# Optimization experiments

Measured on AMD Instinct MI355X. Metric: run time of the kernel, lower is better.

The kernel has to match this reference:

```python
import jax, jax.numpy as jnp
import numpy as np

EPS = 1e-5

def _layer_norm(x, g, b):
    mu = jnp.mean(x, axis=-1, keepdims=True)
    var = jnp.mean(jnp.square(x - mu), axis=-1, keepdims=True)
    return (x - mu) * jax.lax.rsqrt(var + EPS) * g + b

def setup_inputs() -> dict:
    key = jax.random.key(0)
    ks = jax.random.split(key, 12)
    B, N, K = 1, 4096, 64
    TD, P = 384, 128   # token_dim, pair_dim
    H = 2 * P          # transition hidden (expansion_factor_transition=2)
    x = jax.random.normal(ks[0], (B, N, TD), dtype=jnp.float32)
    pair_rep = jax.random.normal(ks[1], (B, N, K, P), dtype=jnp.float32)
    mask = jax.random.uniform(ks[2], (B, N)) > 0.1          # mostly valid residues
    neighbor_idx = jax.random.randint(ks[3], (B, N, K), 0, N, dtype=jnp.int32)
    slot_valid = jax.random.uniform(ks[4], (B, N, K)) > 0.1
    s = 0.02
    params = {
        'ln_g': jnp.ones((TD,), jnp.float32),
        'ln_b': jnp.zeros((TD,), jnp.float32),
        'Wx': jax.random.normal(ks[5], (TD, 2 * P), jnp.float32) * s,
        't_g': jnp.ones((P,), jnp.float32),
        't_b': jnp.zeros((P,), jnp.float32),
        'W1': jax.random.normal(ks[6], (P, H), jnp.float32) * s,
        'b1': jnp.zeros((H,), jnp.float32),
        'W2': jax.random.normal(ks[7], (H, P), jnp.float32) * s,
        'b2': jnp.zeros((P,), jnp.float32),
    }
    return dict(x=x, pair_rep=pair_rep, mask=mask, neighbor_idx=neighbor_idx,
                slot_valid=slot_valid, **params)

def _pair_transition(z, pair_mask, t_g, t_b, W1, b1, W2, b2):
    # OpenFold PairTransition: LN -> Linear -> ReLU -> Linear -> *mask
    h = _layer_norm(z, t_g, t_b)
    h = jax.nn.relu(jnp.einsum('bnkp,ph->bnkh', h, W1) + b1)
    out = jnp.einsum('bnkh,hp->bnkp', h, W2) + b2
    return out * pair_mask[..., None]

def reference(x, pair_rep, mask, neighbor_idx, slot_valid,
              ln_g, ln_b, Wx, t_g, t_b, W1, b1, W2, b2):
    B, N, K, P = pair_rep.shape
    mf = mask.astype(x.dtype)
    xm = x * mf[..., None]
    proj = jnp.einsum('bnt,tp->bnp', _layer_norm(xm, ln_g, ln_b), Wx)  # [B,N,2P]
    xp1, xp2 = proj[..., :P], proj[..., P:]
    flat_idx = neighbor_idx.reshape(B, N * K)
    # gather neighbor projections: xp1_j[b,n,k] = xp1[b, neighbor_idx[b,n,k]]
    xp1_j = jnp.take_along_axis(xp1, flat_idx[..., None], axis=1).reshape(B, N, K, P)
    nbr_valid = jnp.take_along_axis(mask, flat_idx, axis=1).reshape(B, N, K)
    pair_mask = (mask[:, :, None] & nbr_valid & slot_valid).astype(pair_rep.dtype)
    pair_rep = (pair_rep + xp2[:, :, None, :] + xp1_j) * pair_mask[..., None]
    pair_rep = pair_rep + _pair_transition(pair_rep, pair_mask, t_g, t_b, W1, b1, W2, b2)
    pair_rep = pair_rep * pair_mask[..., None]
    return pair_rep
```

## Files before the change

kernel.cpp:

```cpp
#include <hip/hip_runtime.h>
#include <stdint.h>

#define N_TOK 4096
#define TD 384
#define KNB 64
#define PD 128
#define HD 256
#define NPROJ 256
#define RPB 32
#define TPB_LN 16
#define TILES_PER_BLK 8

#define CAN_LN_G 0
#define CAN_LN_B 384
#define CAN_WX   768
#define CAN_T_G  99072
#define CAN_T_B  99200
#define CAN_W1   99328
#define CAN_B1   132096
#define CAN_W2   132352
#define CAN_B2   165120
#define CAN_TOTAL 165248

#define BW_OFF   663552
#define WXT_OFF  0
#define W1T_OFF  98304
#define W2T_OFF  131072
#define BW_TOTAL 163840
#define PROJ_OFF (1 << 20)

typedef __attribute__((ext_vector_type(8))) short bf16x8;
typedef __attribute__((ext_vector_type(4))) short s16x4;
typedef __attribute__((ext_vector_type(4))) float f32x4;
typedef __attribute__((ext_vector_type(2))) unsigned int u32x2;
typedef __attribute__((ext_vector_type(4))) unsigned int u32x4;

static __device__ __forceinline__ float bf2f(unsigned short u) {
    return __uint_as_float(((unsigned int)u) << 16);
}
static __device__ __forceinline__ unsigned short f2bf(float f) {
    unsigned int x = __float_as_uint(f);
    return (unsigned short)((x + 0x7FFFu + ((x >> 16) & 1u)) >> 16);
}
static __device__ __forceinline__ float loadf(const void* p, int mode, int i) {
    return mode ? bf2f(((const unsigned short*)p)[i]) : ((const float*)p)[i];
}
static __device__ __forceinline__ unsigned int flag_word(const void* p, int mode, int i) {
    if (mode == 0) return ((const unsigned int*)p)[i];
    if (mode == 1) return (unsigned int)((const unsigned char*)p)[i];
    if (mode == 2) return (unsigned int)((const unsigned short*)p)[i];
    return ((const unsigned int*)p)[i];
}
static __device__ __forceinline__ bool plaus16(unsigned int h) {
    if (h == 0u) return true;
    unsigned int e = (h >> 7) & 0xFFu;
    return (e >= 0x60u && e <= 0x9Fu);
}

__global__ __launch_bounds__(256) void detect_kernel(
        const void* __restrict__ x, const void* __restrict__ pair_rep,
        const void* __restrict__ mask, const void* __restrict__ slot,
        int* __restrict__ flags) {
    const int t = threadIdx.x;
    const int wave = t >> 6, lane = t & 63;
    if (wave < 2) {
        const unsigned int* w = (const unsigned int*)(wave == 0 ? x : pair_rep);
        unsigned int v = w[lane];
        bool pl = plaus16(v & 0xFFFFu) && plaus16(v >> 16);
        unsigned long long b = __ballot(pl);
        if (lane == 0) flags[2 + wave] = (__popcll(b) >= 56) ? 1 : 0;
    } else {
        const unsigned int* w = (const unsigned int*)(wave == 2 ? mask : slot);
        bool ok01 = true, okbf = true, anybf_lo = false;
        #pragma unroll
        for (int j = 0; j < 4; ++j) {
            unsigned int v = w[lane * 4 + j];
            if (v > 1u) ok01 = false;
            unsigned int h0 = v & 0xFFFFu, h1 = v >> 16;
            if (!(h0 == 0u || h0 == 0x3F80u)) okbf = false;
            if (!(h1 == 0u || h1 == 0x3F80u)) okbf = false;
            if (h0 == 0x3F80u) anybf_lo = true;
        }
        unsigned long long b01 = __ballot(ok01);
        unsigned long long bbf = __ballot(okbf);
        unsigned long long bev = __ballot(anybf_lo);
        if (lane == 0) {
            int mode;
            if (b01 == ~0ull) mode = 0;
            else if (bbf == ~0ull) mode = (bev != 0ull) ? 2 : 3;
            else mode = 1;
            flags[wave - 2] = mode;
        }
    }
}

__global__ __launch_bounds__(256) void prep_kernel(
        const void* p0, const void* p1, const void* p2, const void* p3,
        const void* p4, const void* p5, const void* p6, const void* p7,
        const void* p8, const int* __restrict__ flags,
        float* __restrict__ dstf, short* __restrict__ dstb) {
    const int mode = flags[2];
    int e = blockIdx.x * 256 + threadIdx.x;
    if (e < CAN_TOTAL) {
        const int offs[9] = {CAN_LN_G, CAN_LN_B, CAN_WX, CAN_T_G, CAN_T_B,
                             CAN_W1, CAN_B1, CAN_W2, CAN_B2};
        int s = 0;
        #pragma unroll
        for (int i = 1; i < 9; ++i) if (e >= offs[i]) s = i;
        const int local = e - offs[s];
        const void* p = (s == 0) ? p0 : (s == 1) ? p1 : (s == 2) ? p2 :
                        (s == 3) ? p3 : (s == 4) ? p4 : (s == 5) ? p5 :
                        (s == 6) ? p6 : (s == 7) ? p7 : p8;
        dstf[e] = loadf(p, mode, local);
    } else {
        int e2 = e - CAN_TOTAL;
        if (e2 >= BW_TOTAL) return;
        int src; const void* p;
        if (e2 < W1T_OFF)      { int n = e2 / TD, k = e2 - n * TD;           p = p2; src = k * NPROJ + n; }
        else if (e2 < W2T_OFF) { int l = e2 - W1T_OFF; int n = l >> 7, k = l & 127; p = p5; src = k * HD + n; }
        else                   { int l = e2 - W2T_OFF; int n = l >> 8, k = l & 255; p = p7; src = k * PD + n; }
        dstb[e2] = (short)f2bf(loadf(p, mode, src));
    }
}

__global__ __launch_bounds__(256) void ln_proj_mfma(
        const void* __restrict__ x,
        const float* __restrict__ canon,
        const short* __restrict__ wxt,
        const int* __restrict__ flags,
        unsigned short* __restrict__ projb) {
    __shared__ __align__(16) short xnb[TPB_LN][TD + 8];
    const int t = threadIdx.x, wv = t >> 6, lane = t & 63;
    const int tok0 = blockIdx.x * TPB_LN;
    const int xm = flags[2];

    float g[6], bv[6];
    #pragma unroll
    for (int j = 0; j < 6; ++j) {
        g[j]  = canon[CAN_LN_G + lane + 64 * j];
        bv[j] = canon[CAN_LN_B + lane + 64 * j];
    }
    #pragma unroll
    for (int rr = 0; rr < TPB_LN / 4; ++rr) {
        const int r = wv * (TPB_LN / 4) + rr;
        float v[6], s = 0.f, sq = 0.f;
        #pragma unroll
        for (int j = 0; j < 6; ++j) {
            v[j] = loadf(x, xm, (tok0 + r) * TD + lane + 64 * j);
            s += v[j]; sq += v[j] * v[j];
        }
        #pragma unroll
        for (int off = 32; off > 0; off >>= 1) {
            s += __shfl_down(s, off); sq += __shfl_down(sq, off);
        }
        s = __shfl(s, 0); sq = __shfl(sq, 0);
        const float mu = s * (1.f / TD);
        const float var = sq * (1.f / TD) - mu * mu;
        const float rs = rsqrtf(var + 1e-5f);
        #pragma unroll
        for (int j = 0; j < 6; ++j)
            xnb[r][lane + 64 * j] = (short)f2bf((v[j] - mu) * rs * g[j] + bv[j]);
    }
    __syncthreads();

    const int qr = lane >> 4, ln16 = lane & 15;
    const int n0 = wv * 64;
    f32x4 acc[4];
    #pragma unroll
    for (int nt = 0; nt < 4; ++nt) acc[nt] = f32x4{0.f, 0.f, 0.f, 0.f};
    #pragma unroll
    for (int ks = 0; ks < 12; ++ks) {
        const int k0 = ks * 32 + qr * 8;
        bf16x8 a = *(const bf16x8*)&xnb[ln16][k0];
        #pragma unroll
        for (int nt = 0; nt < 4; ++nt) {
            bf16x8 b = *(const bf16x8*)(wxt + (n0 + nt * 16 + ln16) * TD + k0);
            acc[nt] = __builtin_amdgcn_mfma_f32_16x16x32_bf16(a, b, acc[nt], 0, 0, 0);
        }
    }
    #pragma unroll
    for (int nt = 0; nt < 4; ++nt) {
        const int c = n0 + nt * 16 + ln16;
        #pragma unroll
        for (int r = 0; r < 4; ++r)
            projb[(tok0 + qr * 4 + r) * NPROJ + c] = f2bf(acc[nt][r]);
    }
}

__global__ __launch_bounds__(256, 2) void pair_kernel(
        const void* __restrict__ pair_rep,
        const void* __restrict__ mask,
        const int*  __restrict__ nbr,
        const void* __restrict__ slot,
        const float* __restrict__ canon,
        const short* __restrict__ w1t,
        const short* __restrict__ w2t,
        const unsigned short* __restrict__ projb,
        const int* __restrict__ flags,
        float* __restrict__ out) {
    union ZU {
        short znb[RPB][PD + 8];
        float ol[RPB][PD + 4];
    };
    __shared__ __align__(16) ZU U;
    __shared__ __align__(16) short Hb[RPB][HD + 8];
    __shared__ float pmf2[2][RPB];

    const int t = threadIdx.x;
    const int wv = t >> 6, lane = t & 63, qr = lane >> 4, ln16 = lane & 15;
    const int lr = t >> 5;
    const int c4 = t & 31;
    const int mmode = flags[0], smode = flags[1], prm = flags[3];

    bf16x8 bw1[16];
    bf16x8 bw2[16];
    #pragma unroll
    for (int ks = 0; ks < 4; ++ks)
        #pragma unroll
        for (int nt = 0; nt < 4; ++nt)
            bw1[ks * 4 + nt] = *(const bf16x8*)(
                w1t + (wv * 64 + nt * 16 + ln16) * PD + ks * 32 + qr * 8);
    #pragma unroll
    for (int ks = 0; ks < 8; ++ks)
        #pragma unroll
        for (int nt = 0; nt < 2; ++nt)
            bw2[ks * 2 + nt] = *(const bf16x8*)(
                w2t + (wv * 32 + nt * 16 + ln16) * HD + ks * 32 + qr * 8);

    int idxq[4], mIdx = 0;
    u32x4 pru[4];
    u32x2 pgu[4];
    u32x2 x2u;
    unsigned int wmn = 0, wmi = 0, wsl = 0;

    const int tile0 = blockIdx.x * TILES_PER_BLK;

    {
        const int row0 = tile0 * RPB, n = row0 >> 6, k0 = row0 & (KNB - 1);
        #pragma unroll
        for (int q = 0; q < 4; ++q) idxq[q] = nbr[n * KNB + k0 + 8 * q + lr];
        x2u = *(const u32x2*)(projb + n * NPROJ + PD + 4 * c4);
        #pragma unroll
        for (int q = 0; q < 4; ++q)
            pgu[q] = *(const u32x2*)(projb + idxq[q] * NPROJ + 4 * c4);
        if (prm) {
            const unsigned short* pr = (const unsigned short*)pair_rep;
            #pragma unroll
            for (int q = 0; q < 4; ++q) {
                u32x2 v = __builtin_nontemporal_load(
                    (const u32x2*)(pr + (row0 + 8 * q + lr) * PD + 4 * c4));
                pru[q][0] = v[0]; pru[q][1] = v[1];
            }
        } else {
            const float* pr = (const float*)pair_rep;
            #pragma unroll
            for (int q = 0; q < 4; ++q)
                pru[q] = __builtin_nontemporal_load(
                    (const u32x4*)(pr + (row0 + 8 * q + lr) * PD + 4 * c4));
        }
        if (t < RPB) {
            mIdx = nbr[n * KNB + k0 + t];
            wmn = flag_word(mask, mmode, n);
            wmi = flag_word(mask, mmode, mIdx);
            wsl = flag_word(slot, smode, n * KNB + k0 + t);
            pmf2[0][t] = (wmn && wmi && wsl) ? 1.f : 0.f;
        }
    }

    #pragma unroll 1
    for (int i = 0; i < TILES_PER_BLK; ++i) {
        const int tile = tile0 + i;
        const int cur = i & 1, nxt = cur ^ 1;
        const int row0 = tile * RPB;
        const int tn = (i + 1 < TILES_PER_BLK) ? tile + 1 : tile;
        const int row0n = tn * RPB, nn = row0n >> 6, k0n = row0n & (KNB - 1);

        __syncthreads();

        f32x4 zq[4];
        {
            float x2v[4];
            x2v[0] = bf2f((unsigned short)(x2u[0] & 0xFFFFu));
            x2v[1] = bf2f((unsigned short)(x2u[0] >> 16));
            x2v[2] = bf2f((unsigned short)(x2u[1] & 0xFFFFu));
            x2v[3] = bf2f((unsigned short)(x2u[1] >> 16));
            #pragma unroll
            for (int q = 0; q < 4; ++q) {
                const int row = 8 * q + lr;
                const float pm = pmf2[cur][row];
                float a[4], gg[4];
                gg[0] = bf2f((unsigned short)(pgu[q][0] & 0xFFFFu));
                gg[1] = bf2f((unsigned short)(pgu[q][0] >> 16));
                gg[2] = bf2f((unsigned short)(pgu[q][1] & 0xFFFFu));
                gg[3] = bf2f((unsigned short)(pgu[q][1] >> 16));
                if (prm) {
                    a[0] = bf2f((unsigned short)(pru[q][0] & 0xFFFFu));
                    a[1] = bf2f((unsigned short)(pru[q][0] >> 16));
                    a[2] = bf2f((unsigned short)(pru[q][1] & 0xFFFFu));
                    a[3] = bf2f((unsigned short)(pru[q][1] >> 16));
                } else {
                    a[0] = __uint_as_float(pru[q][0]);
                    a[1] = __uint_as_float(pru[q][1]);
                    a[2] = __uint_as_float(pru[q][2]);
                    a[3] = __uint_as_float(pru[q][3]);
                }
                s16x4 zs;
                #pragma unroll
                for (int e = 0; e < 4; ++e) {
                    const float z = (a[e] + x2v[e] + gg[e]) * pm;
                    zq[q][e] = z;
                    zs[e] = (short)f2bf(z);
                }
                *(s16x4*)&U.znb[row][4 * c4] = zs;
            }
        }

        #pragma unroll
        for (int q = 0; q < 4; ++q) idxq[q] = nbr[nn * KNB + k0n + 8 * q + lr];
        if (t < RPB) mIdx = nbr[nn * KNB + k0n + t];

        __syncthreads();

        {
            const float g0 = canon[CAN_T_G + lane], g1 = canon[CAN_T_G + lane + 64];
            const float b0 = canon[CAN_T_B + lane], b1v = canon[CAN_T_B + lane + 64];
            #pragma unroll
            for (int rr = 0; rr < 8; ++rr) {
                const int r = wv * 8 + rr;
                const float a0 = bf2f((unsigned short)U.znb[r][lane]);
                const float a1 = bf2f((unsigned short)U.znb[r][lane + 64]);
                float s = a0 + a1, sq = a0 * a0 + a1 * a1;
                #pragma unroll
                for (int off = 32; off > 0; off >>= 1) {
                    s += __shfl_down(s, off); sq += __shfl_down(sq, off);
                }
                s = __shfl(s, 0); sq = __shfl(sq, 0);
                const float mu = s * (1.f / PD);
                const float var = sq * (1.f / PD) - mu * mu;
                const float rs = rsqrtf(var + 1e-5f);
                U.znb[r][lane]      = (short)f2bf((a0 - mu) * rs * g0 + b0);
                U.znb[r][lane + 64] = (short)f2bf((a1 - mu) * rs * g1 + b1v);
            }
        }
        __syncthreads();

        {
            f32x4 acc1[2][4];
            #pragma unroll
            for (int mt = 0; mt < 2; ++mt)
                #pragma unroll
                for (int nt = 0; nt < 4; ++nt) acc1[mt][nt] = f32x4{0.f, 0.f, 0.f, 0.f};
            #pragma unroll
            for (int ks = 0; ks < 4; ++ks) {
                const int k0 = ks * 32 + qr * 8;
                bf16x8 a0 = *(const bf16x8*)&U.znb[ln16][k0];
                bf16x8 a1 = *(const bf16x8*)&U.znb[16 + ln16][k0];
                #pragma unroll
                for (int nt = 0; nt < 4; ++nt) {
                    acc1[0][nt] = __builtin_amdgcn_mfma_f32_16x16x32_bf16(a0, bw1[ks * 4 + nt], acc1[0][nt], 0, 0, 0);
                    acc1[1][nt] = __builtin_amdgcn_mfma_f32_16x16x32_bf16(a1, bw1[ks * 4 + nt], acc1[1][nt], 0, 0, 0);
                }
            }
            const int n0 = wv * 64;
            #pragma unroll
            for (int nt = 0; nt < 4; ++nt) {
                const int c = n0 + nt * 16 + ln16;
                const float bb = canon[CAN_B1 + c];
                #pragma unroll
                for (int mt = 0; mt < 2; ++mt)
                    #pragma unroll
                    for (int r = 0; r < 4; ++r) {
                        const float h = acc1[mt][nt][r] + bb;
                        Hb[mt * 16 + qr * 4 + r][c] = (short)f2bf(h > 0.f ? h : 0.f);
                    }
            }
        }
        __syncthreads();

        x2u = *(const u32x2*)(projb + nn * NPROJ + PD + 4 * c4);
        #pragma unroll
        for (int q = 0; q < 4; ++q)
            pgu[q] = *(const u32x2*)(projb + idxq[q] * NPROJ + 4 * c4);
        if (prm) {
            const unsigned short* pr = (const unsigned short*)pair_rep;
            #pragma unroll
            for (int q = 0; q < 4; ++q) {
                u32x2 v = __builtin_nontemporal_load(
                    (const u32x2*)(pr + (row0n + 8 * q + lr) * PD + 4 * c4));
                pru[q][0] = v[0]; pru[q][1] = v[1];
            }
        } else {
            const float* pr = (const float*)pair_rep;
            #pragma unroll
            for (int q = 0; q < 4; ++q)
                pru[q] = __builtin_nontemporal_load(
                    (const u32x4*)(pr + (row0n + 8 * q + lr) * PD + 4 * c4));
        }
        if (t < RPB) {
            wmn = flag_word(mask, mmode, nn);
            wmi = flag_word(mask, mmode, mIdx);
            wsl = flag_word(slot, smode, nn * KNB + k0n + t);
        }

        {
            f32x4 acc2[2][2];
            #pragma unroll
            for (int mt = 0; mt < 2; ++mt)
                #pragma unroll
                for (int nt = 0; nt < 2; ++nt) acc2[mt][nt] = f32x4{0.f, 0.f, 0.f, 0.f};
            #pragma unroll
            for (int ks = 0; ks < 8; ++ks) {
                const int k0 = ks * 32 + qr * 8;
                bf16x8 a0 = *(const bf16x8*)&Hb[ln16][k0];
                bf16x8 a1 = *(const bf16x8*)&Hb[16 + ln16][k0];
                #pragma unroll
                for (int nt = 0; nt < 2; ++nt) {
                    acc2[0][nt] = __builtin_amdgcn_mfma_f32_16x16x32_bf16(a0, bw2[ks * 2 + nt], acc2[0][nt], 0, 0, 0);
                    acc2[1][nt] = __builtin_amdgcn_mfma_f32_16x16x32_bf16(a1, bw2[ks * 2 + nt], acc2[1][nt], 0, 0, 0);
                }
            }
            const int p0w = wv * 32;
            #pragma unroll
            for (int nt = 0; nt < 2; ++nt) {
                const int p = p0w + nt * 16 + ln16;
                const float bb = canon[CAN_B2 + p];
                #pragma unroll
                for (int mt = 0; mt < 2; ++mt)
                    #pragma unroll
                    for (int r = 0; r < 4; ++r) {
                        const int row = mt * 16 + qr * 4 + r;
                        const float pm = pmf2[cur][row];
                        U.ol[row][p] = (acc2[mt][nt][r] + bb) * pm;
                    }
            }
        }
        if (t < RPB) pmf2[nxt][t] = (wmn && wmi && wsl) ? 1.f : 0.f;

        __syncthreads();

        #pragma unroll
        for (int q = 0; q < 4; ++q) {
            const int row = 8 * q + lr;
            f32x4 o = *(const f32x4*)&U.ol[row][4 * c4];
            f32x4 ov = zq[q] + o;
            __builtin_nontemporal_store(ov, (f32x4*)&out[(row0 + row) * PD + 4 * c4]);
        }
    }
}

extern "C" void kernel_launch(void* const* d_in, const int* in_sizes, int n_in,
                              void* d_out, int out_size, void* d_ws, size_t ws_size,
                              hipStream_t stream) {
    const void* x        = d_in[0];
    const void* pair_rep = d_in[1];
    const void* mask     = d_in[2];
    const int*  nbr      = (const int*)d_in[3];
    const void* slot     = d_in[4];
    float* out = (float*)d_out;

    int*   flags = (int*)d_ws;
    float* canon = (float*)((char*)d_ws + 64);
    short* bw    = (short*)((char*)d_ws + BW_OFF);
    const short* wxt = bw + WXT_OFF;
    const short* w1t = bw + W1T_OFF;
    const short* w2t = bw + W2T_OFF;
    unsigned short* projb = (unsigned short*)((char*)d_ws + PROJ_OFF);

    detect_kernel<<<1, 256, 0, stream>>>(x, pair_rep, mask, slot, flags);
    prep_kernel<<<(CAN_TOTAL + BW_TOTAL + 255) / 256, 256, 0, stream>>>(
        d_in[5], d_in[6], d_in[7], d_in[8], d_in[9], d_in[10], d_in[11],
        d_in[12], d_in[13], flags, canon, bw);
    ln_proj_mfma<<<N_TOK / TPB_LN, 256, 0, stream>>>(x, canon, wxt, flags, projb);
    pair_kernel<<<(N_TOK * KNB) / (RPB * TILES_PER_BLK), 256, 0, stream>>>(
        pair_rep, mask, nbr, slot, canon, w1t, w2t, projb, flags, out);
}
```

Baseline: 346.9 us.

## Fuse pair LayerNorm into z-construction via half-wave shuffle reductions

The pair LayerNorm statistics are now computed in registers as each row's z is built, reducing across the 32 lanes that own a row with xor-shuffles, and the normalized bf16 values are written straight to shared memory. This removes one shared-memory round trip of z and one barrier per tile. The z and output staging buffers are split out of their union so the barrier at the top of each tile can be dropped, which costs extra LDS per block and may reduce occupancy. Stats are now taken from fp32 z rather than bf16-rounded z.

```diff
diff --git a/kernel.cpp b/kernel.cpp
--- a/kernel.cpp
+++ b/kernel.cpp
@@ -198,11 +198,8 @@
         const unsigned short* __restrict__ projb,
         const int* __restrict__ flags,
         float* __restrict__ out) {
-    union ZU {
-        short znb[RPB][PD + 8];
-        float ol[RPB][PD + 4];
-    };
-    __shared__ __align__(16) ZU U;
+    __shared__ __align__(16) short znb[RPB][PD + 8];
+    __shared__ __align__(16) float ol[RPB][PD + 4];
     __shared__ __align__(16) short Hb[RPB][HD + 8];
     __shared__ float pmf2[2][RPB];
 
@@ -226,6 +223,13 @@
         for (int nt = 0; nt < 2; ++nt)
             bw2[ks * 2 + nt] = *(const bf16x8*)(
                 w2t + (wv * 32 + nt * 16 + ln16) * HD + ks * 32 + qr * 8);
+
+    float tg[4], tb[4];
+    #pragma unroll
+    for (int e = 0; e < 4; ++e) {
+        tg[e] = canon[CAN_T_G + 4 * c4 + e];
+        tb[e] = canon[CAN_T_B + 4 * c4 + e];
+    }
 
     int idxq[4], mIdx = 0;
     u32x4 pru[4];
@@ -266,6 +270,7 @@
             pmf2[0][t] = (wmn && wmi && wsl) ? 1.f : 0.f;
         }
     }
+    __syncthreads();
 
     #pragma unroll 1
     for (int i = 0; i < TILES_PER_BLK; ++i) {
@@ -274,8 +279,6 @@
         const int row0 = tile * RPB;
         const int tn = (i + 1 < TILES_PER_BLK) ? tile + 1 : tile;
         const int row0n = tn * RPB, nn = row0n >> 6, k0n = row0n & (KNB - 1);
-
-        __syncthreads();
 
         f32x4 zq[4];
         {
@@ -304,44 +307,33 @@
                     a[2] = __uint_as_float(pru[q][2]);
                     a[3] = __uint_as_float(pru[q][3]);
                 }
-                s16x4 zs;
+                float s = 0.f, sq = 0.f;
                 #pragma unroll
                 for (int e = 0; e < 4; ++e) {
                     const float z = (a[e] + x2v[e] + gg[e]) * pm;
                     zq[q][e] = z;
-                    zs[e] = (short)f2bf(z);
+                    s += z; sq += z * z;
                 }
-                *(s16x4*)&U.znb[row][4 * c4] = zs;
-            }
-        }
-
-        #pragma unroll
-        for (int q = 0; q < 4; ++q) idxq[q] = nbr[nn * KNB + k0n + 8 * q + lr];
-        if (t < RPB) mIdx = nbr[nn * KNB + k0n + t];
-
-        __syncthreads();
-
-        {
-            const float g0 = canon[CAN_T_G + lane], g1 = canon[CAN_T_G + lane + 64];
-            const float b0 = canon[CAN_T_B + lane], b1v = canon[CAN_T_B + lane + 64];
-            #pragma unroll
-            for (int rr = 0; rr < 8; ++rr) {
-                const int r = wv * 8 + rr;
-                const float a0 = bf2f((unsigned short)U.znb[r][lane]);
-                const float a1 = bf2f((unsigned short)U.znb[r][lane + 64]);
-                float s = a0 + a1, sq = a0 * a0 + a1 * a1;
-                #pragma unroll
-                for (int off = 32; off > 0; off >>= 1) {
-                    s += __shfl_down(s, off); sq += __shfl_down(sq, off);
+                #pragma unroll
+                for (int off = 16; off > 0; off >>= 1) {
+                    s  += __shfl_xor(s, off);
+                    sq += __shfl_xor(sq, off);
                 }
-                s = __shfl(s, 0); sq = __shfl(sq, 0);
                 const float mu = s * (1.f / PD);
                 const float var = sq * (1.f / PD) - mu * mu;
                 const float rs = rsqrtf(var + 1e-5f);
-                U.znb[r][lane]      = (short)f2bf((a0 - mu) * rs * g0 + b0);
-                U.znb[r][lane + 64] = (short)f2bf((a1 - mu) * rs * g1 + b1v);
-            }
-        }
+                s16x4 zs;
+                #pragma unroll
+                for (int e = 0; e < 4; ++e)
+                    zs[e] = (short)f2bf((zq[q][e] - mu) * rs * tg[e] + tb[e]);
+                *(s16x4*)&znb[row][4 * c4] = zs;
+            }
+        }
+
+        #pragma unroll
+        for (int q = 0; q < 4; ++q) idxq[q] = nbr[nn * KNB + k0n + 8 * q + lr];
+        if (t < RPB) mIdx = nbr[nn * KNB + k0n + t];
+
         __syncthreads();
 
         {
@@ -353,8 +345,8 @@
             #pragma unroll
             for (int ks = 0; ks < 4; ++ks) {
                 const int k0 = ks * 32 + qr * 8;
-                bf16x8 a0 = *(const bf16x8*)&U.znb[ln16][k0];
-                bf16x8 a1 = *(const bf16x8*)&U.znb[16 + ln16][k0];
+                bf16x8 a0 = *(const bf16x8*)&znb[ln16][k0];
+                bf16x8 a1 = *(const bf16x8*)&znb[16 + ln16][k0];
                 #pragma unroll
                 for (int nt = 0; nt < 4; ++nt) {
                     acc1[0][nt] = __builtin_amdgcn_mfma_f32_16x16x32_bf16(a0, bw1[ks * 4 + nt], acc1[0][nt], 0, 0, 0);
@@ -430,7 +422,7 @@
                     for (int r = 0; r < 4; ++r) {
                         const int row = mt * 16 + qr * 4 + r;
                         const float pm = pmf2[cur][row];
-                        U.ol[row][p] = (acc2[mt][nt][r] + bb) * pm;
+                        ol[row][p] = (acc2[mt][nt][r] + bb) * pm;
                     }
             }
         }
@@ -441,7 +433,7 @@
         #pragma unroll
         for (int q = 0; q < 4; ++q) {
             const int row = 8 * q + lr;
-            f32x4 o = *(const f32x4*)&U.ol[row][4 * c4];
+            f32x4 o = *(const f32x4*)&ol[row][4 * c4];
             f32x4 ov = zq[q] + o;
             __builtin_nontemporal_store(ov, (f32x4*)&out[(row0 + row) * PD + 4 * c4]);
         }
```

After: 329.6 us. 5.0% less time.
